# Kernel optimization log

Hardware: AMD Instinct MI355X
Metric: run time of the kernel (lower is better)

The kernel has to match this reference:

```python
import jax, jax.numpy as jnp
import numpy as np

B, M, QH, D = 2, 4096, 16, 192   # batch, q_len, q heads, qk head dim
N, VD = 255, 128                 # compressed kv blocks, v head dim


def setup_inputs() -> dict:
    key = jax.random.key(0)
    kq, kk, kv = jax.random.split(key, 3)
    return {
        "q": jax.random.normal(kq, (B, M, QH, D), dtype=jnp.float32),
        "k": jax.random.normal(kk, (B, N, QH, D), dtype=jnp.float32),
        "v": jax.random.normal(kv, (B, N, QH, VD), dtype=jnp.float32),
        "real_length": M,
        "kernel_size": 32,
        "stride": 16,
    }


def reference(q, k, v, real_length, kernel_size, stride):
    # q: [b, m, h, d]; k: [b, n, h, d]; v: [b, n, h, vd]
    b, m, h, d = q.shape
    n = k.shape[1]
    sm_scale = d ** (-0.5)  # config.sm_scale is None -> default scale

    # scores: [b, h, m, n]
    s = jnp.einsum("bmhd,bnhd->bhmn", q, k) * sm_scale

    # block-stride causal mask: query i may attend to compressed block j only
    # if the block's last covered position (j*stride + kernel_size - 1) <= i
    q_idx = jnp.arange(m, dtype=jnp.int32)          # m == real_length prefill path
    k_idx = jnp.arange(n, dtype=jnp.int32) * stride + kernel_size - 1
    mask = q_idx[:, None] < k_idx[None, :]          # [m, n] True -> masked
    s = jnp.where(mask[None, None], jnp.finfo(s.dtype).min, s)

    # fp32 softmax then cast back (matches softmax(dtype=torch.float32).to(dtype))
    p = jax.nn.softmax(s.astype(jnp.float32), axis=-1).astype(s.dtype)

    # o: [b, m, h, vd] (already transposed back as in the torch return)
    o = jnp.einsum("bhmn,bnhd->bmhd", p, v)

    # queries earlier than the first complete block produce zero output
    o = jnp.where((q_idx < kernel_size - 1)[None, :, None, None], 0.0, o)
    return (o, p)
```

## Files before the change

kernel.cpp:

```cpp
#include <hip/hip_runtime.h>
#include <hip/hip_bf16.h>
#include <stdint.h>
#include <math.h>

typedef __attribute__((ext_vector_type(8))) __bf16 bf16x8;
typedef __attribute__((ext_vector_type(4))) __bf16 bf16x4;
typedef __attribute__((ext_vector_type(4))) float f32x4;
typedef __attribute__((ext_vector_type(4), aligned(4))) float f32x4u;
typedef __attribute__((ext_vector_type(2), aligned(4))) float f32x2u;

#define B_   2
#define M_   4096
#define QH_  16
#define D_   192
#define N_   255
#define VD_  128


__global__ __launch_bounds__(256) void prep_k(const float* __restrict__ k,
                                              __bf16* __restrict__ kimg) {
    const int chunk = blockIdx.x * 256 + threadIdx.x;
    const int wc   = chunk % 384;
    const int tile = chunk / 384;
    const int c16  = wc & 15;
    const int gq   = (wc >> 4) & 3;
    const int s    = wc >> 6;
    const int jt   = tile & 15;
    const int bh   = tile >> 4;
    const int b    = bh >> 4, h = bh & 15;
    const int n    = jt * 16 + c16;
    bf16x8 out;
    if (n < N_) {
        const float* src = k + ((size_t)((b * N_ + n) * QH_ + h)) * D_ + s * 32 + gq * 8;
        f32x4 s0 = *(const f32x4*)src;
        f32x4 s1 = *(const f32x4*)(src + 4);
        out[0]=(__bf16)s0[0]; out[1]=(__bf16)s0[1]; out[2]=(__bf16)s0[2]; out[3]=(__bf16)s0[3];
        out[4]=(__bf16)s1[0]; out[5]=(__bf16)s1[1]; out[6]=(__bf16)s1[2]; out[7]=(__bf16)s1[3];
    } else {
        #pragma unroll
        for (int e = 0; e < 8; ++e) out[e] = (__bf16)0.f;
    }
    *(bf16x8*)(kimg + (size_t)chunk * 8) = out;
}

__global__ __launch_bounds__(256) void prep_v(const float* __restrict__ v,
                                              __bf16* __restrict__ vimg) {
    const int chunk = blockIdx.x * 256 + threadIdx.x;
    const int wc  = chunk & 511;
    const int img = chunk >> 9;
    const int c16 = wc & 15;
    const int gq  = (wc >> 4) & 3;
    const int vdt = wc >> 6;
    const int c   = img & 7;
    const int bh  = img >> 3;
    const int b   = bh >> 4, h = bh & 15;
    const int vd  = vdt * 16 + c16;
    const int n0  = c * 32 + gq * 8;
    bf16x8 out;
    #pragma unroll
    for (int t = 0; t < 8; ++t) {
        const int n = n0 + t;
        float val = (n < N_) ? v[((size_t)((b * N_ + n) * QH_ + h)) * VD_ + vd] : 0.f;
        out[t] = (__bf16)val;
    }
    *(bf16x8*)(vimg + (size_t)chunk * 8) = out;
}

__global__ __launch_bounds__(64) void cattn_kernel(
    const float* __restrict__ q, const __bf16* __restrict__ kimg,
    const __bf16* __restrict__ vimg, float* __restrict__ o_out,
    float* __restrict__ p_out)
{
    const float scale = 0.07216878364870322f;
    const int bid  = blockIdx.x;
    const int iw16 = 255 - (bid & 255);
    const int h    = (bid >> 8) & 15;
    const int b    = bid >> 12;
    const int bh   = b * QH_ + h;

    const int lane = threadIdx.x;
    const int g    = lane >> 4;
    const int c16  = lane & 15;
    const int iw   = iw16 << 4;
    const int i    = iw + c16;
    const bool dead = (i < 31);

    bf16x8 bq[6];
    {
        const float* qrow = q + ((size_t)((b * M_ + i) * QH_ + h)) * D_;
        #pragma unroll
        for (int s = 0; s < 6; ++s) {
            f32x4 q0 = __builtin_nontemporal_load((const f32x4*)(qrow + s * 32 + g * 8));
            f32x4 q1 = __builtin_nontemporal_load((const f32x4*)(qrow + s * 32 + g * 8 + 4));
            bf16x8 a;
            a[0]=(__bf16)q0[0]; a[1]=(__bf16)q0[1]; a[2]=(__bf16)q0[2]; a[3]=(__bf16)q0[3];
            a[4]=(__bf16)q1[0]; a[5]=(__bf16)q1[1]; a[6]=(__bf16)q1[2]; a[7]=(__bf16)q1[3];
            bq[s] = a;
        }
    }

    int jt_any = (iw >= 16) ? ((iw - 16) >> 8) : -1;
    if (jt_any > 15) jt_any = 15;

    f32x4 sacc[16];
    #pragma unroll
    for (int jt = 0; jt < 16; ++jt)
        sacc[jt] = (f32x4){-INFINITY, -INFINITY, -INFINITY, -INFINITY};

    const __bf16* kbh = kimg + (size_t)(bh * 16) * 3072 + g * 128 + c16 * 8;

    bf16x8 kfA[6], kfB[6];
    if (jt_any >= 0) {
        #pragma unroll
        for (int s = 0; s < 6; ++s) kfA[s] = *(const bf16x8*)(kbh + s * 512);
    }

#define QK_STEP(JT, KCUR, KNXT)                                                \
    if ((JT) <= jt_any) {                                                      \
        if ((JT) + 1 <= jt_any) {                                              \
            const __bf16* kr = kbh + (size_t)((JT) + 1) * 3072;                \
            _Pragma("unroll")                                                  \
            for (int s = 0; s < 6; ++s) KNXT[s] = *(const bf16x8*)(kr + s*512);\
        }                                                                      \
        f32x4 acc = {0.f, 0.f, 0.f, 0.f};                                      \
        _Pragma("unroll")                                                      \
        for (int s = 0; s < 6; ++s)                                            \
            acc = __builtin_amdgcn_mfma_f32_16x16x32_bf16(KCUR[s], bq[s], acc, 0, 0, 0); \
        _Pragma("unroll")                                                      \
        for (int r = 0; r < 4; ++r) {                                          \
            const int n = (JT) * 16 + g * 4 + r;                               \
            const bool live = (n < N_) && (i >= 16 * n + 31);                  \
            acc[r] = live ? acc[r] * scale : ((n < N_) ? -1e30f : -INFINITY);  \
        }                                                                      \
        sacc[(JT)] = acc;                                                      \
    }

    QK_STEP(0,  kfA, kfB)  QK_STEP(1,  kfB, kfA)
    QK_STEP(2,  kfA, kfB)  QK_STEP(3,  kfB, kfA)
    QK_STEP(4,  kfA, kfB)  QK_STEP(5,  kfB, kfA)
    QK_STEP(6,  kfA, kfB)  QK_STEP(7,  kfB, kfA)
    QK_STEP(8,  kfA, kfB)  QK_STEP(9,  kfB, kfA)
    QK_STEP(10, kfA, kfB)  QK_STEP(11, kfB, kfA)
    QK_STEP(12, kfA, kfB)  QK_STEP(13, kfB, kfA)
    QK_STEP(14, kfA, kfB)  QK_STEP(15, kfB, kfA)
#undef QK_STEP

    float m = -INFINITY;
    #pragma unroll
    for (int jt = 0; jt < 16; ++jt) {
        #pragma unroll
        for (int r = 0; r < 4; ++r) m = fmaxf(m, sacc[jt][r]);
    }
    m = fmaxf(m, __shfl_xor(m, 16));
    m = fmaxf(m, __shfl_xor(m, 32));
    float sum = 0.f;
    #pragma unroll
    for (int jt = 0; jt < 16; ++jt) {
        #pragma unroll
        for (int r = 0; r < 4; ++r) {
            float e = __expf(sacc[jt][r] - m);
            sacc[jt][r] = e;
            sum += e;
        }
    }
    sum += __shfl_xor(sum, 16);
    sum += __shfl_xor(sum, 32);
    const float inv_l = 1.0f / sum;
    const float u255  = 0.00392156862745098f;

    unsigned long long pnp[16];
    float* prow = p_out + (size_t)(bh * M_ + i) * N_ + g * 4;
    #pragma unroll
    for (int jt = 0; jt < 16; ++jt) {
        f32x4 px;
        #pragma unroll
        for (int r = 0; r < 4; ++r)
            px[r] = dead ? u255 : sacc[jt][r] * inv_l;
        if (jt == 15 && g == 3) {
            f32x2u p2; p2[0] = px[0]; p2[1] = px[1];
            *(f32x2u*)(prow + 15 * 16) = p2;
            prow[15 * 16 + 2] = px[2];
        } else {
            *(f32x4u*)(prow + jt * 16) = *(f32x4u*)&px;
        }
        union { bf16x4 v; unsigned long long u; } pk;
        #pragma unroll
        for (int r = 0; r < 4; ++r) pk.v[r] = (__bf16)px[r];
        pnp[jt] = pk.u;
    }

    f32x4 oacc[8];
    #pragma unroll
    for (int t = 0; t < 8; ++t) oacc[t] = (f32x4){0.f, 0.f, 0.f, 0.f};

    const int c_lim = (jt_any < 0) ? 0 : ((jt_any + 2) >> 1);
    const __bf16* vth = vimg + (size_t)(bh * 8) * 4096 + g * 128 + c16 * 8;
    const int src0 = ((g & 1) << 5) + c16;
    const int src1 = src0 + 16;
    const bool selhi = (g >= 2);

    bf16x8 vbA[8], vbB[8];
    if (0 < c_lim) {
        #pragma unroll
        for (int t = 0; t < 8; ++t) vbA[t] = *(const bf16x8*)(vth + t * 512);
    }

#define PV_STEP(C, VBc, VBn)                                                   \
    if ((C) < c_lim) {                                                         \
        if ((C) + 1 < c_lim) {                                                 \
            const __bf16* vc = vth + (size_t)((C) + 1) * 4096;                 \
            _Pragma("unroll")                                                  \
            for (int t = 0; t < 8; ++t) VBn[t] = *(const bf16x8*)(vc + t*512); \
        }                                                                      \
        unsigned long long lo0 = __shfl(pnp[2 * (C)],     src0);               \
        unsigned long long lo1 = __shfl(pnp[2 * (C) + 1], src0);               \
        unsigned long long hi0 = __shfl(pnp[2 * (C)],     src1);               \
        unsigned long long hi1 = __shfl(pnp[2 * (C) + 1], src1);               \
        union { struct { unsigned long long x, y; } u; bf16x8 v; } pa8;        \
        pa8.u.x = selhi ? lo1 : lo0;                                           \
        pa8.u.y = selhi ? hi1 : hi0;                                           \
        const bf16x8 pa = pa8.v;                                               \
        _Pragma("unroll")                                                      \
        for (int vdt = 0; vdt < 8; ++vdt)                                      \
            oacc[vdt] = __builtin_amdgcn_mfma_f32_16x16x32_bf16(VBc[vdt], pa, oacc[vdt], 0, 0, 0); \
    }

    PV_STEP(0, vbA, vbB)
    PV_STEP(1, vbB, vbA)
    PV_STEP(2, vbA, vbB)
    PV_STEP(3, vbB, vbA)
    PV_STEP(4, vbA, vbB)
    PV_STEP(5, vbB, vbA)
    PV_STEP(6, vbA, vbB)
    PV_STEP(7, vbB, vbA)
#undef PV_STEP

    float* orow = o_out + ((size_t)(b * M_ + i) * QH_ + h) * VD_ + g * 4;
    #pragma unroll
    for (int vdt = 0; vdt < 8; ++vdt) {
        f32x4 ov;
        #pragma unroll
        for (int r = 0; r < 4; ++r) ov[r] = dead ? 0.f : oacc[vdt][r];
        *(f32x4*)(orow + vdt * 16) = ov;
    }
}

extern "C" void kernel_launch(void* const* d_in, const int* in_sizes, int n_in,
                              void* d_out, int out_size, void* d_ws, size_t ws_size,
                              hipStream_t stream) {
    (void)in_sizes; (void)n_in; (void)ws_size; (void)out_size;
    const float* q = (const float*)d_in[0];
    const float* k = (const float*)d_in[1];
    const float* v = (const float*)d_in[2];
    float* o_out = (float*)d_out;
    float* p_out = o_out + (size_t)B_ * M_ * QH_ * VD_;

    __bf16* kimg = (__bf16*)d_ws;
    __bf16* vimg = kimg + (size_t)32 * 16 * 3072;

    prep_k<<<dim3(768), dim3(256), 0, stream>>>(k, kimg);
    prep_v<<<dim3(512), dim3(256), 0, stream>>>(v, vimg);

    dim3 grid(B_ * QH_ * 256);
    dim3 block(64);
    cattn_kernel<<<grid, block, 0, stream>>>(q, kimg, vimg, o_out, p_out);
}
```

Baseline: 104.9 us.

## Drop max-subtraction softmax, fuse exp into QK loop, defer normalization to output

```diff
diff --git a/kernel.cpp b/kernel.cpp
--- a/kernel.cpp
+++ b/kernel.cpp
@@ -102,80 +102,63 @@
     int jt_any = (iw >= 16) ? ((iw - 16) >> 8) : -1;
     if (jt_any > 15) jt_any = 15;
 
-    f32x4 sacc[16];
-    #pragma unroll
-    for (int jt = 0; jt < 16; ++jt)
-        sacc[jt] = (f32x4){-INFINITY, -INFINITY, -INFINITY, -INFINITY};
-
+    unsigned long long pnp[16];
+    #pragma unroll
+    for (int jt = 0; jt < 16; ++jt) pnp[jt] = 0ULL;
+
+    float s0 = 0.f, s1 = 0.f, s2 = 0.f, s3 = 0.f;
     const __bf16* kbh = kimg + (size_t)(bh * 16) * 3072 + g * 128 + c16 * 8;
 
-    bf16x8 kfA[6], kfB[6];
-    if (jt_any >= 0) {
-        #pragma unroll
-        for (int s = 0; s < 6; ++s) kfA[s] = *(const bf16x8*)(kbh + s * 512);
-    }
-
-#define QK_STEP(JT, KCUR, KNXT)                                                \
+#define QK_STEP(JT)                                                            \
     if ((JT) <= jt_any) {                                                      \
-        if ((JT) + 1 <= jt_any) {                                              \
-            const __bf16* kr = kbh + (size_t)((JT) + 1) * 3072;                \
-            _Pragma("unroll")                                                  \
-            for (int s = 0; s < 6; ++s) KNXT[s] = *(const bf16x8*)(kr + s*512);\
-        }                                                                      \
+        const __bf16* kr = kbh + (size_t)(JT) * 3072;                          \
+        bf16x8 kf0 = *(const bf16x8*)(kr);                                     \
+        bf16x8 kf1 = *(const bf16x8*)(kr + 512);                               \
+        bf16x8 kf2 = *(const bf16x8*)(kr + 1024);                              \
+        bf16x8 kf3 = *(const bf16x8*)(kr + 1536);                              \
+        bf16x8 kf4 = *(const bf16x8*)(kr + 2048);                              \
+        bf16x8 kf5 = *(const bf16x8*)(kr + 2560);                              \
         f32x4 acc = {0.f, 0.f, 0.f, 0.f};                                      \
-        _Pragma("unroll")                                                      \
-        for (int s = 0; s < 6; ++s)                                            \
-            acc = __builtin_amdgcn_mfma_f32_16x16x32_bf16(KCUR[s], bq[s], acc, 0, 0, 0); \
-        _Pragma("unroll")                                                      \
-        for (int r = 0; r < 4; ++r) {                                          \
-            const int n = (JT) * 16 + g * 4 + r;                               \
-            const bool live = (n < N_) && (i >= 16 * n + 31);                  \
-            acc[r] = live ? acc[r] * scale : ((n < N_) ? -1e30f : -INFINITY);  \
-        }                                                                      \
-        sacc[(JT)] = acc;                                                      \
-    }
-
-    QK_STEP(0,  kfA, kfB)  QK_STEP(1,  kfB, kfA)
-    QK_STEP(2,  kfA, kfB)  QK_STEP(3,  kfB, kfA)
-    QK_STEP(4,  kfA, kfB)  QK_STEP(5,  kfB, kfA)
-    QK_STEP(6,  kfA, kfB)  QK_STEP(7,  kfB, kfA)
-    QK_STEP(8,  kfA, kfB)  QK_STEP(9,  kfB, kfA)
-    QK_STEP(10, kfA, kfB)  QK_STEP(11, kfB, kfA)
-    QK_STEP(12, kfA, kfB)  QK_STEP(13, kfB, kfA)
-    QK_STEP(14, kfA, kfB)  QK_STEP(15, kfB, kfA)
+        acc = __builtin_amdgcn_mfma_f32_16x16x32_bf16(kf0, bq[0], acc, 0, 0, 0); \
+        acc = __builtin_amdgcn_mfma_f32_16x16x32_bf16(kf1, bq[1], acc, 0, 0, 0); \
+        acc = __builtin_amdgcn_mfma_f32_16x16x32_bf16(kf2, bq[2], acc, 0, 0, 0); \
+        acc = __builtin_amdgcn_mfma_f32_16x16x32_bf16(kf3, bq[3], acc, 0, 0, 0); \
+        acc = __builtin_amdgcn_mfma_f32_16x16x32_bf16(kf4, bq[4], acc, 0, 0, 0); \
+        acc = __builtin_amdgcn_mfma_f32_16x16x32_bf16(kf5, bq[5], acc, 0, 0, 0); \
+        const int n0 = (JT) * 16 + g * 4;                                      \
+                      \
+        float e0 = ((n0 + 0 < N_) && (i >= 16 * (n0 + 0) + 31)) ? __expf(acc[0] * scale) : 0.f; \
+        float e1 = ((n0 + 1 < N_) && (i >= 16 * (n0 + 1) + 31)) ? __expf(acc[1] * scale) : 0.f; \
+        float e2 = ((n0 + 2 < N_) && (i >= 16 * (n0 + 2) + 31)) ? __expf(acc[2] * scale) : 0.f; \
+        float e3 = ((n0 + 3 < N_) && (i >= 16 * (n0 + 3) + 31)) ? __expf(acc[3] * scale) : 0.f; \
+        s0 += e0; s1 += e1; s2 += e2; s3 += e3;                                \
+        union { bf16x4 v; unsigned long long u; } pk;                          \
+        pk.v[0] = (__bf16)e0; pk.v[1] = (__bf16)e1;                            \
+        pk.v[2] = (__bf16)e2; pk.v[3] = (__bf16)e3;                            \
+        pnp[(JT)] = pk.u;                                                      \
+    }
+
+    QK_STEP(0)  QK_STEP(1)  QK_STEP(2)  QK_STEP(3)
+    QK_STEP(4)  QK_STEP(5)  QK_STEP(6)  QK_STEP(7)
+    QK_STEP(8)  QK_STEP(9)  QK_STEP(10) QK_STEP(11)
+    QK_STEP(12) QK_STEP(13) QK_STEP(14) QK_STEP(15)
 #undef QK_STEP
 
-    float m = -INFINITY;
-    #pragma unroll
-    for (int jt = 0; jt < 16; ++jt) {
-        #pragma unroll
-        for (int r = 0; r < 4; ++r) m = fmaxf(m, sacc[jt][r]);
-    }
-    m = fmaxf(m, __shfl_xor(m, 16));
-    m = fmaxf(m, __shfl_xor(m, 32));
-    float sum = 0.f;
-    #pragma unroll
-    for (int jt = 0; jt < 16; ++jt) {
-        #pragma unroll
-        for (int r = 0; r < 4; ++r) {
-            float e = __expf(sacc[jt][r] - m);
-            sacc[jt][r] = e;
-            sum += e;
-        }
-    }
+    float sum = (s0 + s1) + (s2 + s3);
     sum += __shfl_xor(sum, 16);
     sum += __shfl_xor(sum, 32);
     const float inv_l = 1.0f / sum;
     const float u255  = 0.00392156862745098f;
 
-    unsigned long long pnp[16];
     float* prow = p_out + (size_t)(bh * M_ + i) * N_ + g * 4;
     #pragma unroll
     for (int jt = 0; jt < 16; ++jt) {
+        union { bf16x4 v; unsigned long long u; } pk;
+        pk.u = pnp[jt];
         f32x4 px;
         #pragma unroll
         for (int r = 0; r < 4; ++r)
-            px[r] = dead ? u255 : sacc[jt][r] * inv_l;
+            px[r] = dead ? u255 : (float)pk.v[r] * inv_l;
         if (jt == 15 && g == 3) {
             f32x2u p2; p2[0] = px[0]; p2[1] = px[1];
             *(f32x2u*)(prow + 15 * 16) = p2;
@@ -183,10 +166,6 @@
         } else {
             *(f32x4u*)(prow + jt * 16) = *(f32x4u*)&px;
         }
-        union { bf16x4 v; unsigned long long u; } pk;
-        #pragma unroll
-        for (int r = 0; r < 4; ++r) pk.v[r] = (__bf16)px[r];
-        pnp[jt] = pk.u;
     }
 
     f32x4 oacc[8];
@@ -199,19 +178,17 @@
     const int src1 = src0 + 16;
     const bool selhi = (g >= 2);
 
-    bf16x8 vbA[8], vbB[8];
-    if (0 < c_lim) {
-        #pragma unroll
-        for (int t = 0; t < 8; ++t) vbA[t] = *(const bf16x8*)(vth + t * 512);
-    }
-
-#define PV_STEP(C, VBc, VBn)                                                   \
+#define PV_STEP(C)                                                             \
     if ((C) < c_lim) {                                                         \
-        if ((C) + 1 < c_lim) {                                                 \
-            const __bf16* vc = vth + (size_t)((C) + 1) * 4096;                 \
-            _Pragma("unroll")                                                  \
-            for (int t = 0; t < 8; ++t) VBn[t] = *(const bf16x8*)(vc + t*512); \
-        }                                                                      \
+        const __bf16* vc = vth + (size_t)(C) * 4096;                           \
+        bf16x8 vb0 = *(const bf16x8*)(vc);                                     \
+        bf16x8 vb1 = *(const bf16x8*)(vc + 512);                               \
+        bf16x8 vb2 = *(const bf16x8*)(vc + 1024);                              \
+        bf16x8 vb3 = *(const bf16x8*)(vc + 1536);                              \
+        bf16x8 vb4 = *(const bf16x8*)(vc + 2048);                              \
+        bf16x8 vb5 = *(const bf16x8*)(vc + 2560);                              \
+        bf16x8 vb6 = *(const bf16x8*)(vc + 3072);                              \
+        bf16x8 vb7 = *(const bf16x8*)(vc + 3584);                              \
         unsigned long long lo0 = __shfl(pnp[2 * (C)],     src0);               \
         unsigned long long lo1 = __shfl(pnp[2 * (C) + 1], src0);               \
         unsigned long long hi0 = __shfl(pnp[2 * (C)],     src1);               \
@@ -220,19 +197,18 @@
         pa8.u.x = selhi ? lo1 : lo0;                                           \
         pa8.u.y = selhi ? hi1 : hi0;                                           \
         const bf16x8 pa = pa8.v;                                               \
-        _Pragma("unroll")                                                      \
-        for (int vdt = 0; vdt < 8; ++vdt)                                      \
-            oacc[vdt] = __builtin_amdgcn_mfma_f32_16x16x32_bf16(VBc[vdt], pa, oacc[vdt], 0, 0, 0); \
-    }
-
-    PV_STEP(0, vbA, vbB)
-    PV_STEP(1, vbB, vbA)
-    PV_STEP(2, vbA, vbB)
-    PV_STEP(3, vbB, vbA)
-    PV_STEP(4, vbA, vbB)
-    PV_STEP(5, vbB, vbA)
-    PV_STEP(6, vbA, vbB)
-    PV_STEP(7, vbB, vbA)
+        oacc[0] = __builtin_amdgcn_mfma_f32_16x16x32_bf16(vb0, pa, oacc[0], 0, 0, 0); \
+        oacc[1] = __builtin_amdgcn_mfma_f32_16x16x32_bf16(vb1, pa, oacc[1], 0, 0, 0); \
+        oacc[2] = __builtin_amdgcn_mfma_f32_16x16x32_bf16(vb2, pa, oacc[2], 0, 0, 0); \
+        oacc[3] = __builtin_amdgcn_mfma_f32_16x16x32_bf16(vb3, pa, oacc[3], 0, 0, 0); \
+        oacc[4] = __builtin_amdgcn_mfma_f32_16x16x32_bf16(vb4, pa, oacc[4], 0, 0, 0); \
+        oacc[5] = __builtin_amdgcn_mfma_f32_16x16x32_bf16(vb5, pa, oacc[5], 0, 0, 0); \
+        oacc[6] = __builtin_amdgcn_mfma_f32_16x16x32_bf16(vb6, pa, oacc[6], 0, 0, 0); \
+        oacc[7] = __builtin_amdgcn_mfma_f32_16x16x32_bf16(vb7, pa, oacc[7], 0, 0, 0); \
+    }
+
+    PV_STEP(0) PV_STEP(1) PV_STEP(2) PV_STEP(3)
+    PV_STEP(4) PV_STEP(5) PV_STEP(6) PV_STEP(7)
 #undef PV_STEP
 
     float* orow = o_out + ((size_t)(b * M_ + i) * QH_ + h) * VD_ + g * 4;
@@ -240,8 +216,8 @@
     for (int vdt = 0; vdt < 8; ++vdt) {
         f32x4 ov;
         #pragma unroll
-        for (int r = 0; r < 4; ++r) ov[r] = dead ? 0.f : oacc[vdt][r];
-        *(f32x4*)(orow + vdt * 16) = ov;
+        for (int r = 0; r < 4; ++r) ov[r] = dead ? 0.f : oacc[vdt][r] * inv_l;
+        __builtin_nontemporal_store(ov, (f32x4*)(orow + vdt * 16));
     }
 }
 
```

Result: slower. 140.9 us (+34.3%).
